# Kernel optimization log

Measured on AMD Instinct MI355X. Metric: run time of the kernel, lower is better.

## Reference

```python
import jax, jax.numpy as jnp
import numpy as np

N_NODES = 524288
N_EDGES = 786432
NUM_GRAPHS = 8192
NUM_NODE_TYPES = 16
NODE_DIM = 256
EDGE_DIM = 128
OUT_DIM = 1


def setup_inputs() -> dict:
    key = jax.random.key(0)
    ks = jax.random.split(key, 12)
    h_node = jax.random.uniform(ks[0], (N_NODES, NUM_NODE_TYPES), dtype=jnp.float32)
    pos_node = jax.random.normal(ks[1], (N_NODES, 3), dtype=jnp.float32)
    batch_node = jnp.sort(jax.random.randint(ks[2], (N_NODES,), 0, NUM_GRAPHS)).astype(jnp.int64)
    edge_index = jax.random.randint(ks[3], (2, N_EDGES), 0, N_NODES).astype(jnp.int64)
    batch_edge = jnp.sort(jax.random.randint(ks[4], (N_EDGES,), 0, NUM_GRAPHS)).astype(jnp.int64)
    s = 0.05
    W_node = jax.random.normal(ks[5], (NUM_NODE_TYPES, NODE_DIM), dtype=jnp.float32) * s
    W_edge = jax.random.normal(ks[6], (2 * NUM_NODE_TYPES, EDGE_DIM), dtype=jnp.float32) * s
    H = NODE_DIM + EDGE_DIM
    W1 = jax.random.normal(ks[7], (H, H), dtype=jnp.float32) * s
    b1 = jnp.zeros((H,), dtype=jnp.float32)
    W2 = jax.random.normal(ks[8], (H, OUT_DIM), dtype=jnp.float32) * s
    b2 = jnp.zeros((OUT_DIM,), dtype=jnp.float32)
    return {"h_node": h_node, "pos_node": pos_node, "batch_node": batch_node,
            "edge_index": edge_index, "batch_edge": batch_edge,
            "W_node": W_node, "W_edge": W_edge, "W1": W1, "b1": b1, "W2": W2, "b2": b2}


def _segment_mean(x, seg_ids, num_segments):
    # fused replacement for the original per-graph boolean-mask loop:
    # h[seg==k].mean(0) for all k, via one scatter-add + count normalize
    sums = jax.ops.segment_sum(x, seg_ids, num_segments=num_segments)
    cnts = jax.ops.segment_sum(jnp.ones((x.shape[0],), x.dtype), seg_ids, num_segments=num_segments)
    return sums / jnp.maximum(cnts, 1.0)[:, None]


def reference(h_node, pos_node, batch_node, edge_index, batch_edge,
              W_node, W_edge, W1, b1, W2, b2):
    # h_edge = cat(h_node[src], h_node[dst])  -> [E, 2*num_node_types]
    h_edge_raw = jnp.concatenate([h_node[edge_index[0]], h_node[edge_index[1]]], axis=-1)
    # num_timesteps == 0 path: plain embedders, no time embedding
    hn = h_node @ W_node          # [N, node_dim]
    he = h_edge_raw @ W_edge      # [E, edge_dim]
    # encoder treated as identity (NodeEdgeNet not in scope); pooling is the target op
    node_mean = _segment_mean(hn, batch_node, NUM_GRAPHS)  # [G, node_dim]
    edge_mean = _segment_mean(he, batch_edge, NUM_GRAPHS)  # [G, edge_dim]
    h_sub = jnp.concatenate([node_mean, edge_mean], axis=-1)  # [G, node_dim+edge_dim]
    # final MLP (num_layer=2): Linear -> ReLU -> Linear
    pred = jax.nn.relu(h_sub @ W1 + b1) @ W2 + b2  # [G, 1]
    return pred
```

## Files before the change

kernel.cpp:

```cpp
#include <hip/hip_runtime.h>

#define N_NODES_C   524288
#define N_EDGES_C   786432
#define NUM_GRAPHS_C 8192
#define NT 16
#define NODE_DIM_C 256
#define EDGE_DIM_C 128
#define HDIM 384
#define KC 48

#define START_BLOCKS 65
#define FOLD_BLOCKS  72

#define WS_SN    0
#define WS_SE    65536
#define WS_NM    131072
#define WS_EM    655360
#define WS_WC    1703936

__device__ __forceinline__ int lower_bound_i32(const int* __restrict__ a, int n, int key) {
    int lo = 0, hi = n;
    while (lo < hi) {
        int mid = (lo + hi) >> 1;
        if (a[mid] < key) lo = mid + 1; else hi = mid;
    }
    return lo;
}

__global__ __launch_bounds__(256) void kp_prep(
    const int* __restrict__ bnode, const int* __restrict__ bedge,
    const float* __restrict__ Wn, const float* __restrict__ We,
    const float* __restrict__ W1,
    int* __restrict__ sn, int* __restrict__ se, float* __restrict__ Wc) {
    int blk = blockIdx.x;
    if (blk < START_BLOCKS) {
        int t = blk * 256 + threadIdx.x;
        if (t < NUM_GRAPHS_C + 1) {
            sn[t] = lower_bound_i32(bnode, N_NODES_C, t);
        } else if (t < 2 * (NUM_GRAPHS_C + 1)) {
            se[t - (NUM_GRAPHS_C + 1)] = lower_bound_i32(bedge, N_EDGES_C, t - (NUM_GRAPHS_C + 1));
        }
    } else {
        int o = (blk - START_BLOCKS) * 256 + threadIdx.x;
        if (o >= KC * HDIM) return;
        int k = o / HDIM, j = o % HDIM;
        float acc = 0.f;
        if (k < NT) {
            const float* wr = &Wn[k * NODE_DIM_C];
            #pragma unroll 16
            for (int kk = 0; kk < NODE_DIM_C; ++kk)
                acc = fmaf(wr[kk], W1[(size_t)kk * HDIM + j], acc);
        } else {
            const float* wr = &We[(k - NT) * EDGE_DIM_C];
            #pragma unroll 16
            for (int kk = 0; kk < EDGE_DIM_C; ++kk)
                acc = fmaf(wr[kk], W1[(size_t)(NODE_DIM_C + kk) * HDIM + j], acc);
        }
        Wc[o] = acc;
    }
}

__device__ __forceinline__ void f4_shfl_xor_add(float4& a, int mask) {
    a.x += __shfl_xor(a.x, mask, 64);
    a.y += __shfl_xor(a.y, mask, 64);
    a.z += __shfl_xor(a.z, mask, 64);
    a.w += __shfl_xor(a.w, mask, 64);
}

__global__ __launch_bounds__(256) void km_means(
    const float* __restrict__ h_node, const int* __restrict__ sn,
    const int* __restrict__ se,
    const int* __restrict__ esrc, const int* __restrict__ edst,
    float* __restrict__ nm, float* __restrict__ em) {
    int wave = threadIdx.x >> 6;
    int lane = threadIdx.x & 63;
    const float4* h4 = (const float4*)h_node;

    if (blockIdx.x < 2048) {
        int g = blockIdx.x * 4 + wave;
        int s = se[g], e = se[g + 1];
        int p  = lane >> 5;
        int sl = lane & 31;
        const int* __restrict__ idxp = p ? edst : esrc;
        float4 a0 = make_float4(0.f, 0.f, 0.f, 0.f);
        float4 a1 = a0, a2 = a0, a3 = a0;
        for (int i = s + sl; i < e; i += 32) {
            const float4* row = h4 + (size_t)idxp[i] * 4;
            float4 v0 = row[0], v1 = row[1], v2 = row[2], v3 = row[3];
            a0.x += v0.x; a0.y += v0.y; a0.z += v0.z; a0.w += v0.w;
            a1.x += v1.x; a1.y += v1.y; a1.z += v1.z; a1.w += v1.w;
            a2.x += v2.x; a2.y += v2.y; a2.z += v2.z; a2.w += v2.w;
            a3.x += v3.x; a3.y += v3.y; a3.z += v3.z; a3.w += v3.w;
        }
        #pragma unroll
        for (int mask = 1; mask < 32; mask <<= 1) {
            f4_shfl_xor_add(a0, mask);
            f4_shfl_xor_add(a1, mask);
            f4_shfl_xor_add(a2, mask);
            f4_shfl_xor_add(a3, mask);
        }
        if (sl == 0) {
            float inv = 1.f / fmaxf((float)(e - s), 1.f);
            float4* emo = ((float4*)em) + (size_t)g * 8 + p * 4;
            emo[0] = make_float4(a0.x * inv, a0.y * inv, a0.z * inv, a0.w * inv);
            emo[1] = make_float4(a1.x * inv, a1.y * inv, a1.z * inv, a1.w * inv);
            emo[2] = make_float4(a2.x * inv, a2.y * inv, a2.z * inv, a2.w * inv);
            emo[3] = make_float4(a3.x * inv, a3.y * inv, a3.z * inv, a3.w * inv);
        }
    } else {
        int g = (blockIdx.x - 2048) * 4 + wave;
        int s = sn[g], e = sn[g + 1];
        int row_off = lane >> 2;
        int quad    = lane & 3;
        float4 acc = make_float4(0.f, 0.f, 0.f, 0.f);
        for (int i = s + row_off; i < e; i += 16) {
            float4 v = h4[(size_t)i * 4 + quad];
            acc.x += v.x; acc.y += v.y; acc.z += v.z; acc.w += v.w;
        }
        f4_shfl_xor_add(acc, 4);
        f4_shfl_xor_add(acc, 8);
        f4_shfl_xor_add(acc, 16);
        f4_shfl_xor_add(acc, 32);
        if (row_off == 0) {
            float inv = 1.f / fmaxf((float)(e - s), 1.f);
            ((float4*)nm)[(size_t)g * 4 + quad] =
                make_float4(acc.x * inv, acc.y * inv, acc.z * inv, acc.w * inv);
        }
    }
}

#define GPB 16
__global__ __launch_bounds__(HDIM) void k3_mlp(
    const float* __restrict__ nm, const float* __restrict__ em,
    const float* __restrict__ Wc, const float* __restrict__ b1,
    const float* __restrict__ W2, const float* __restrict__ b2,
    float* __restrict__ pred) {
    int j = threadIdx.x;
    float wc[KC];
    #pragma unroll
    for (int k = 0; k < KC; ++k) wc[k] = Wc[k * HDIM + j];
    float b1j = b1[j], w2j = W2[j], b20 = b2[0];

    __shared__ float fs[GPB][KC];
    __shared__ float part[GPB][6];
    int g0 = blockIdx.x * GPB;
    #pragma unroll
    for (int t = j; t < GPB * KC; t += HDIM) {
        int g = t / KC, k = t % KC;
        fs[g][k] = (k < NT) ? nm[(size_t)(g0 + g) * NT + k]
                            : em[(size_t)(g0 + g) * 32 + (k - NT)];
    }
    __syncthreads();

    int wave = j >> 6, lane = j & 63;
    for (int g = 0; g < GPB; ++g) {
        float z = b1j;
        #pragma unroll
        for (int k = 0; k < KC; ++k) z = fmaf(fs[g][k], wc[k], z);
        z = fmaxf(z, 0.f);
        float p = z * w2j;
        #pragma unroll
        for (int off = 32; off > 0; off >>= 1) p += __shfl_down(p, off, 64);
        if (lane == 0) part[g][wave] = p;
    }
    __syncthreads();
    if (j < GPB) {
        float sacc = b20;
        #pragma unroll
        for (int w = 0; w < 6; ++w) sacc += part[j][w];
        pred[g0 + j] = sacc;
    }
}

extern "C" void kernel_launch(void* const* d_in, const int* in_sizes, int n_in,
                              void* d_out, int out_size, void* d_ws, size_t ws_size,
                              hipStream_t stream) {
    const float* h_node     = (const float*)d_in[0];
    const int*   batch_node = (const int*)d_in[2];
    const int*   edge_index = (const int*)d_in[3];
    const int*   batch_edge = (const int*)d_in[4];
    const float* W_node     = (const float*)d_in[5];
    const float* W_edge     = (const float*)d_in[6];
    const float* W1         = (const float*)d_in[7];
    const float* b1         = (const float*)d_in[8];
    const float* W2         = (const float*)d_in[9];
    const float* b2         = (const float*)d_in[10];
    float* pred = (float*)d_out;

    char* ws = (char*)d_ws;
    int*   sn = (int*)(ws + WS_SN);
    int*   se = (int*)(ws + WS_SE);
    float* nm = (float*)(ws + WS_NM);
    float* em = (float*)(ws + WS_EM);
    float* Wc = (float*)(ws + WS_WC);

    const int* esrc = edge_index;
    const int* edst = edge_index + N_EDGES_C;

    kp_prep<<<START_BLOCKS + FOLD_BLOCKS, 256, 0, stream>>>(
        batch_node, batch_edge, W_node, W_edge, W1, sn, se, Wc);
    km_means<<<4096, 256, 0, stream>>>(h_node, sn, se, esrc, edst, nm, em);
    k3_mlp<<<NUM_GRAPHS_C / GPB, HDIM, 0, stream>>>(nm, em, Wc, b1, W2, b2, pred);
}
```

Before: 148.5 us.

## Fuse prep and segment-mean kernels, compute bounds per wave, restructure edge gather

Removes the separate prep kernel that wrote segment boundaries to workspace. Each wave now binary-searches its own start and end bounds inline, and the weight fold runs as extra blocks of the same launch, saving one launch and one dependency. The edge gather is remapped so each lane loads one float4 quad per row, two edges in flight with index prefetch, which aims to raise memory-level parallelism with fewer registers. The cost is redundant binary searches per wave and a more serial dependency chain before the gather starts.

After: 148.4 us. Within noise of the previous version (-0.1%).

```diff
diff --git a/kernel.cpp b/kernel.cpp
--- a/kernel.cpp
+++ b/kernel.cpp
@@ -9,14 +9,16 @@
 #define HDIM 384
 #define KC 48
 
-#define START_BLOCKS 65
 #define FOLD_BLOCKS  72
-
-#define WS_SN    0
-#define WS_SE    65536
-#define WS_NM    131072
-#define WS_EM    655360
-#define WS_WC    1703936
+#define EDGE_BLOCKS  2048
+#define NODE_BLOCKS  2048
+#define EDGE_BASE    FOLD_BLOCKS
+#define NODE_BASE    (FOLD_BLOCKS + EDGE_BLOCKS)
+#define TOTAL_BLOCKS (FOLD_BLOCKS + EDGE_BLOCKS + NODE_BLOCKS)
+
+#define WS_NM    0
+#define WS_EM    524288
+#define WS_WC    1572864
 
 __device__ __forceinline__ int lower_bound_i32(const int* __restrict__ a, int n, int key) {
     int lo = 0, hi = n;
@@ -27,21 +29,35 @@
     return lo;
 }
 
-__global__ __launch_bounds__(256) void kp_prep(
+__device__ __forceinline__ void wave_seg_bounds(const int* __restrict__ b, int n,
+                                                int g, int lane, int& s, int& e) {
+    int key = g + ((lane >= 32) ? 1 : 0);
+    int lo = lower_bound_i32(b, n, key);
+    s = __shfl(lo, 0, 64);
+    e = __shfl(lo, 32, 64);
+}
+
+__device__ __forceinline__ void f4_shfl_xor_add(float4& a, int mask) {
+    a.x += __shfl_xor(a.x, mask, 64);
+    a.y += __shfl_xor(a.y, mask, 64);
+    a.z += __shfl_xor(a.z, mask, 64);
+    a.w += __shfl_xor(a.w, mask, 64);
+}
+
+__global__ __launch_bounds__(256) void km_mega(
+    const float* __restrict__ h_node,
     const int* __restrict__ bnode, const int* __restrict__ bedge,
+    const int* __restrict__ esrc, const int* __restrict__ edst,
     const float* __restrict__ Wn, const float* __restrict__ We,
     const float* __restrict__ W1,
-    int* __restrict__ sn, int* __restrict__ se, float* __restrict__ Wc) {
-    int blk = blockIdx.x;
-    if (blk < START_BLOCKS) {
-        int t = blk * 256 + threadIdx.x;
-        if (t < NUM_GRAPHS_C + 1) {
-            sn[t] = lower_bound_i32(bnode, N_NODES_C, t);
-        } else if (t < 2 * (NUM_GRAPHS_C + 1)) {
-            se[t - (NUM_GRAPHS_C + 1)] = lower_bound_i32(bedge, N_EDGES_C, t - (NUM_GRAPHS_C + 1));
-        }
-    } else {
-        int o = (blk - START_BLOCKS) * 256 + threadIdx.x;
+    float* __restrict__ nm, float* __restrict__ em, float* __restrict__ Wc) {
+    int blk  = blockIdx.x;
+    int wave = threadIdx.x >> 6;
+    int lane = threadIdx.x & 63;
+    const float4* h4 = (const float4*)h_node;
+
+    if (blk < FOLD_BLOCKS) {
+        int o = blk * 256 + threadIdx.x;
         if (o >= KC * HDIM) return;
         int k = o / HDIM, j = o % HDIM;
         float acc = 0.f;
@@ -57,59 +73,46 @@
                 acc = fmaf(wr[kk], W1[(size_t)(NODE_DIM_C + kk) * HDIM + j], acc);
         }
         Wc[o] = acc;
-    }
-}
-
-__device__ __forceinline__ void f4_shfl_xor_add(float4& a, int mask) {
-    a.x += __shfl_xor(a.x, mask, 64);
-    a.y += __shfl_xor(a.y, mask, 64);
-    a.z += __shfl_xor(a.z, mask, 64);
-    a.w += __shfl_xor(a.w, mask, 64);
-}
-
-__global__ __launch_bounds__(256) void km_means(
-    const float* __restrict__ h_node, const int* __restrict__ sn,
-    const int* __restrict__ se,
-    const int* __restrict__ esrc, const int* __restrict__ edst,
-    float* __restrict__ nm, float* __restrict__ em) {
-    int wave = threadIdx.x >> 6;
-    int lane = threadIdx.x & 63;
-    const float4* h4 = (const float4*)h_node;
-
-    if (blockIdx.x < 2048) {
-        int g = blockIdx.x * 4 + wave;
-        int s = se[g], e = se[g + 1];
-        int p  = lane >> 5;
-        int sl = lane & 31;
+    } else if (blk < NODE_BASE) {
+        int g = (blk - EDGE_BASE) * 4 + wave;
+        int s, e;
+        wave_seg_bounds(bedge, N_EDGES_C, g, lane, s, e);
+        int eo   = lane >> 3;
+        int p    = (lane >> 2) & 1;
+        int quad = lane & 3;
         const int* __restrict__ idxp = p ? edst : esrc;
-        float4 a0 = make_float4(0.f, 0.f, 0.f, 0.f);
-        float4 a1 = a0, a2 = a0, a3 = a0;
-        for (int i = s + sl; i < e; i += 32) {
-            const float4* row = h4 + (size_t)idxp[i] * 4;
-            float4 v0 = row[0], v1 = row[1], v2 = row[2], v3 = row[3];
-            a0.x += v0.x; a0.y += v0.y; a0.z += v0.z; a0.w += v0.w;
-            a1.x += v1.x; a1.y += v1.y; a1.z += v1.z; a1.w += v1.w;
-            a2.x += v2.x; a2.y += v2.y; a2.z += v2.z; a2.w += v2.w;
-            a3.x += v3.x; a3.y += v3.y; a3.z += v3.z; a3.w += v3.w;
-        }
-        #pragma unroll
-        for (int mask = 1; mask < 32; mask <<= 1) {
-            f4_shfl_xor_add(a0, mask);
-            f4_shfl_xor_add(a1, mask);
-            f4_shfl_xor_add(a2, mask);
-            f4_shfl_xor_add(a3, mask);
-        }
-        if (sl == 0) {
+        float4 accA = make_float4(0.f, 0.f, 0.f, 0.f);
+        float4 accB = accA;
+        int iA = s + eo, iB = s + eo + 8;
+        int nxA = (iA < e) ? idxp[iA] : -1;
+        int nxB = (iB < e) ? idxp[iB] : -1;
+        while (nxB >= 0) {
+            int idxA = nxA, idxB = nxB;
+            iA += 16; iB += 16;
+            nxA = (iA < e) ? idxp[iA] : -1;
+            nxB = (iB < e) ? idxp[iB] : -1;
+            float4 va = h4[(size_t)idxA * 4 + quad];
+            float4 vb = h4[(size_t)idxB * 4 + quad];
+            accA.x += va.x; accA.y += va.y; accA.z += va.z; accA.w += va.w;
+            accB.x += vb.x; accB.y += vb.y; accB.z += vb.z; accB.w += vb.w;
+        }
+        if (nxA >= 0) {
+            float4 v = h4[(size_t)nxA * 4 + quad];
+            accA.x += v.x; accA.y += v.y; accA.z += v.z; accA.w += v.w;
+        }
+        accA.x += accB.x; accA.y += accB.y; accA.z += accB.z; accA.w += accB.w;
+        f4_shfl_xor_add(accA, 8);
+        f4_shfl_xor_add(accA, 16);
+        f4_shfl_xor_add(accA, 32);
+        if (eo == 0) {
             float inv = 1.f / fmaxf((float)(e - s), 1.f);
-            float4* emo = ((float4*)em) + (size_t)g * 8 + p * 4;
-            emo[0] = make_float4(a0.x * inv, a0.y * inv, a0.z * inv, a0.w * inv);
-            emo[1] = make_float4(a1.x * inv, a1.y * inv, a1.z * inv, a1.w * inv);
-            emo[2] = make_float4(a2.x * inv, a2.y * inv, a2.z * inv, a2.w * inv);
-            emo[3] = make_float4(a3.x * inv, a3.y * inv, a3.z * inv, a3.w * inv);
+            ((float4*)em)[(size_t)g * 8 + p * 4 + quad] =
+                make_float4(accA.x * inv, accA.y * inv, accA.z * inv, accA.w * inv);
         }
     } else {
-        int g = (blockIdx.x - 2048) * 4 + wave;
-        int s = sn[g], e = sn[g + 1];
+        int g = (blk - NODE_BASE) * 4 + wave;
+        int s, e;
+        wave_seg_bounds(bnode, N_NODES_C, g, lane, s, e);
         int row_off = lane >> 2;
         int quad    = lane & 3;
         float4 acc = make_float4(0.f, 0.f, 0.f, 0.f);
@@ -188,8 +191,6 @@
     float* pred = (float*)d_out;
 
     char* ws = (char*)d_ws;
-    int*   sn = (int*)(ws + WS_SN);
-    int*   se = (int*)(ws + WS_SE);
     float* nm = (float*)(ws + WS_NM);
     float* em = (float*)(ws + WS_EM);
     float* Wc = (float*)(ws + WS_WC);
@@ -197,8 +198,7 @@
     const int* esrc = edge_index;
     const int* edst = edge_index + N_EDGES_C;
 
-    kp_prep<<<START_BLOCKS + FOLD_BLOCKS, 256, 0, stream>>>(
-        batch_node, batch_edge, W_node, W_edge, W1, sn, se, Wc);
-    km_means<<<4096, 256, 0, stream>>>(h_node, sn, se, esrc, edst, nm, em);
+    km_mega<<<TOTAL_BLOCKS, 256, 0, stream>>>(
+        h_node, batch_node, batch_edge, esrc, edst, W_node, W_edge, W1, nm, em, Wc);
     k3_mlp<<<NUM_GRAPHS_C / GPB, HDIM, 0, stream>>>(nm, em, Wc, b1, W2, b2, pred);
 }
```
